# Kernel optimization log

Hardware: AMD Instinct MI355X
Metric: run time of the kernel (lower is better)

## Reference

```python
import jax, jax.numpy as jnp
import numpy as np

N_NODES = 50000
N_EDGES = 800000
F_IN, F_LAT, F_OUT = 64, 64, 64


def _graph_conv(x, W, b, src, dst, deg_out_isqrt, deg_in_isqrt):
    # DGL GraphConv, norm='both': D_out^{-1/2} scaling on src side,
    # linear transform (mult-first since in_feats >= out_feats),
    # scatter-sum to dst, D_in^{-1/2} scaling on dst side, + bias.
    n = x.shape[0]
    h = (x * deg_out_isqrt[:, None]) @ W              # [N, F_out]
    msg = h[src]                                      # [E, F_out] gather
    agg = jax.ops.segment_sum(msg, dst, num_segments=n)  # [N, F_out] scatter
    return agg * deg_in_isqrt[:, None] + b


def setup_inputs() -> dict:
    key = jax.random.key(0)
    ks = jax.random.split(key, 6)
    x = jax.random.normal(ks[0], (N_NODES, F_IN), dtype=jnp.float32)
    W1 = jax.random.normal(ks[1], (F_IN, F_LAT), dtype=jnp.float32) / np.sqrt(F_IN)
    b1 = jnp.zeros((F_LAT,), dtype=jnp.float32)
    W2 = jax.random.normal(ks[2], (F_LAT, F_OUT), dtype=jnp.float32) / np.sqrt(F_LAT)
    b2 = jnp.zeros((F_OUT,), dtype=jnp.float32)
    src = jax.random.randint(ks[3], (N_EDGES,), 0, N_NODES, dtype=jnp.int32)
    dst = jax.random.randint(ks[4], (N_EDGES,), 0, N_NODES, dtype=jnp.int32)
    return {"x": x, "W1": W1, "b1": b1, "W2": W2, "b2": b2, "src": src, "dst": dst}


def reference(x, W1, b1, W2, b2, src, dst):
    n = x.shape[0]
    ones = jnp.ones((src.shape[0],), dtype=x.dtype)
    deg_out = jax.ops.segment_sum(ones, src, num_segments=n)
    deg_in = jax.ops.segment_sum(ones, dst, num_segments=n)
    deg_out_isqrt = jnp.where(deg_out > 0, jax.lax.rsqrt(jnp.maximum(deg_out, 1.0)), 0.0)
    deg_in_isqrt = jnp.where(deg_in > 0, jax.lax.rsqrt(jnp.maximum(deg_in, 1.0)), 0.0)
    h = _graph_conv(x, W1, b1, src, dst, deg_out_isqrt, deg_in_isqrt)
    h = jax.nn.relu(h)
    out = _graph_conv(h, W2, b2, src, dst, deg_out_isqrt, deg_in_isqrt)
    return out
```

## Files before the change

### kernel.cpp

```cpp
#include <hip/hip_runtime.h>

#define NF 64
#define BC 32
#define RANGE 16384
#define RWORDS (RANGE / 4)

typedef __attribute__((ext_vector_type(8))) short short8;
typedef __attribute__((ext_vector_type(4))) float floatx4;

__device__ __forceinline__ unsigned short f2bf(float f) {
  unsigned int u = __float_as_uint(f);
  return (unsigned short)((u + 0x7fffu + ((u >> 16) & 1u)) >> 16);
}

__global__ __launch_bounds__(512) void hist_kernel(
    const int* __restrict__ src, const int* __restrict__ dst,
    unsigned char* __restrict__ Gout, unsigned char* __restrict__ Gin,
    unsigned char* __restrict__ rank, int n, int nE, int R, int chunk) {
  __shared__ int cnt[RWORDS];
  const int rb = blockIdx.x % (R * BC);
  const int kind = blockIdx.x / (R * BC);
  const int r = rb / BC, b = rb % BC;
  const int r0 = r * RANGE;
  for (int i = threadIdx.x; i < RWORDS; i += 512) cnt[i] = 0;
  __syncthreads();
  const int lo = b * chunk, hi = min(lo + chunk, nE);
  const int* keys = kind ? src : dst;
  const int n4 = (hi > lo) ? ((hi - lo) >> 2) : 0;
  const int4* keys4 = (const int4*)(keys + lo);
  if (kind == 0) {
    for (int i = threadIdx.x; i < n4; i += 512) {
      int4 v = keys4[i];
      int e0 = lo + 4 * i;
      unsigned int k, old, sh;
      k = (unsigned int)(v.x - r0);
      if (k < (unsigned int)RANGE) { sh = (k & 3) * 8; old = atomicAdd(&cnt[k >> 2], 1u << sh); rank[e0 + 0] = (unsigned char)(old >> sh); }
      k = (unsigned int)(v.y - r0);
      if (k < (unsigned int)RANGE) { sh = (k & 3) * 8; old = atomicAdd(&cnt[k >> 2], 1u << sh); rank[e0 + 1] = (unsigned char)(old >> sh); }
      k = (unsigned int)(v.z - r0);
      if (k < (unsigned int)RANGE) { sh = (k & 3) * 8; old = atomicAdd(&cnt[k >> 2], 1u << sh); rank[e0 + 2] = (unsigned char)(old >> sh); }
      k = (unsigned int)(v.w - r0);
      if (k < (unsigned int)RANGE) { sh = (k & 3) * 8; old = atomicAdd(&cnt[k >> 2], 1u << sh); rank[e0 + 3] = (unsigned char)(old >> sh); }
    }
    for (int e = lo + 4 * n4 + threadIdx.x; e < hi; e += 512) {
      unsigned int k = (unsigned int)(keys[e] - r0);
      if (k < (unsigned int)RANGE) {
        unsigned int sh = (k & 3) * 8;
        unsigned int old = atomicAdd(&cnt[k >> 2], 1u << sh);
        rank[e] = (unsigned char)(old >> sh);
      }
    }
    __syncthreads();
    unsigned int* Gw = (unsigned int*)(Gin + (size_t)b * n + r0);
    for (int i = threadIdx.x; i < RWORDS; i += 512)
      if (r0 + 4 * i < n) Gw[i] = (unsigned int)cnt[i];
  } else {
    for (int i = threadIdx.x; i < n4; i += 512) {
      int4 v = keys4[i];
      unsigned int k;
      k = (unsigned int)(v.x - r0);
      if (k < (unsigned int)RANGE) atomicAdd(&cnt[k >> 2], 1u << ((k & 3) * 8));
      k = (unsigned int)(v.y - r0);
      if (k < (unsigned int)RANGE) atomicAdd(&cnt[k >> 2], 1u << ((k & 3) * 8));
      k = (unsigned int)(v.z - r0);
      if (k < (unsigned int)RANGE) atomicAdd(&cnt[k >> 2], 1u << ((k & 3) * 8));
      k = (unsigned int)(v.w - r0);
      if (k < (unsigned int)RANGE) atomicAdd(&cnt[k >> 2], 1u << ((k & 3) * 8));
    }
    for (int e = lo + 4 * n4 + threadIdx.x; e < hi; e += 512) {
      unsigned int k = (unsigned int)(keys[e] - r0);
      if (k < (unsigned int)RANGE) atomicAdd(&cnt[k >> 2], 1u << ((k & 3) * 8));
    }
    __syncthreads();
    unsigned int* Gw = (unsigned int*)(Gout + (size_t)b * n + r0);
    for (int i = threadIdx.x; i < RWORDS; i += 512)
      if (r0 + 4 * i < n) Gw[i] = (unsigned int)cnt[i];
  }
}

__global__ __launch_bounds__(256) void colscan_scan1_kernel(
    unsigned char* __restrict__ Gin, const unsigned char* __restrict__ Gout,
    float* __restrict__ so, float* __restrict__ si,
    int* __restrict__ lscan, int* __restrict__ bsum, int n) {
  __shared__ int s[256];
  const int tid = threadIdx.x;
  const int i = blockIdx.x * 256 + tid;
  int di = 0;
  if (i < n) {
    int base = 0;
    #pragma unroll 8
    for (int b = 0; b < BC; ++b) {
      int c = Gin[(size_t)b * n + i];
      Gin[(size_t)b * n + i] = (unsigned char)base;
      base += c;
    }
    di = base;
    int dsum = 0;
    #pragma unroll 8
    for (int b = 0; b < BC; ++b) dsum += Gout[(size_t)b * n + i];
    si[i] = di > 0 ? rsqrtf((float)di) : 0.f;
    so[i] = dsum > 0 ? rsqrtf((float)dsum) : 0.f;
  }
  s[tid] = di;
  __syncthreads();
  #pragma unroll
  for (int off = 1; off < 256; off <<= 1) {
    int t2 = (tid >= off) ? s[tid - off] : 0;
    __syncthreads();
    s[tid] += t2;
    __syncthreads();
  }
  if (i < n) lscan[i] = s[tid] - di;
  if (tid == 255) bsum[blockIdx.x] = s[255];
}

__global__ __launch_bounds__(256) void scan3_basefill_kernel(
    const int* __restrict__ lscan, const int* __restrict__ bsum,
    const unsigned char* __restrict__ Gin, int* __restrict__ row_start,
    int* __restrict__ base, int n, int nb, int nE) {
  __shared__ int red[256];
  const int tid = threadIdx.x;
  const int c = blockIdx.x / nb;
  const int ib = blockIdx.x % nb;
  red[tid] = (tid < ib) ? bsum[tid] : 0;
  __syncthreads();
  #pragma unroll
  for (int s = 128; s > 0; s >>= 1) {
    if (tid < s) red[tid] += red[tid + s];
    __syncthreads();
  }
  const int off = red[0];
  const int i = ib * 256 + tid;
  if (i < n) {
    const int rs = lscan[i] + off;
    if (c == 0) row_start[i] = rs;
    base[(size_t)c * n + i] = rs + (int)Gin[(size_t)c * n + i];
  }
  if (c == 0 && ib == 0 && tid == 0) row_start[n] = nE;
}

__device__ __forceinline__ void mfma_gemm_core(
    const unsigned short* __restrict__ Ab, const unsigned short* __restrict__ Wt,
    unsigned short* __restrict__ H, int row0, int n, int t) {
  const int w = t >> 6, lane = t & 63;
  const int quad = lane >> 4, l15 = lane & 15;
  const short8 a0 = *(const short8*)&Ab[(w * 16 + l15) * 72 + quad * 8];
  const short8 a1 = *(const short8*)&Ab[(w * 16 + l15) * 72 + 32 + quad * 8];
  #pragma unroll
  for (int cg = 0; cg < 4; ++cg) {
    const short8 b0 = *(const short8*)&Wt[(cg * 16 + l15) * 72 + quad * 8];
    const short8 b1 = *(const short8*)&Wt[(cg * 16 + l15) * 72 + 32 + quad * 8];
    floatx4 acc = {0.f, 0.f, 0.f, 0.f};
    acc = __builtin_amdgcn_mfma_f32_16x16x32_bf16(a0, b0, acc, 0, 0, 0);
    acc = __builtin_amdgcn_mfma_f32_16x16x32_bf16(a1, b1, acc, 0, 0, 0);
    #pragma unroll
    for (int reg = 0; reg < 4; ++reg) {
      int grow = row0 + w * 16 + quad * 4 + reg;
      if (grow < n) H[(size_t)grow * NF + cg * 16 + l15] = f2bf(acc[reg]);
    }
  }
}

__device__ __forceinline__ void stage_wt(
    const float* __restrict__ W, unsigned short* __restrict__ Wt, int t) {
  #pragma unroll
  for (int i = 0; i < 16; ++i) {
    int idx = t + 256 * i;
    int k = idx >> 6, j = idx & 63;
    Wt[j * 72 + k] = f2bf(W[idx]);
  }
}

__global__ __launch_bounds__(256) void place_gemm1_kernel(
    const float* __restrict__ A, const float* __restrict__ so,
    const float* __restrict__ W, unsigned short* __restrict__ H, int n, int ggrid,
    const int* __restrict__ src, const int* __restrict__ dst,
    const unsigned char* __restrict__ rank, const int* __restrict__ base,
    unsigned short* __restrict__ sorted, int nE, int chunk) {
  __shared__ __align__(16) unsigned short Ab[64 * 72];
  __shared__ __align__(16) unsigned short Wt[64 * 72];
  const int t = threadIdx.x;
  if ((int)blockIdx.x >= ggrid) {
    int e = (blockIdx.x - ggrid) * 256 + t;
    if (e < nE) {
      int d = dst[e];
      int b = e / chunk;
      sorted[base[(size_t)b * n + d] + (int)rank[e]] = (unsigned short)src[e];
    }
    return;
  }
  stage_wt(W, Wt, t);
  const int row0 = blockIdx.x * 64;
  #pragma unroll
  for (int i = 0; i < 4; ++i) {
    int idx = t + 256 * i;
    int r = idx >> 4, c4 = idx & 15;
    int gr = row0 + r;
    float4 v = {0.f, 0.f, 0.f, 0.f};
    float s = 0.f;
    if (gr < n) {
      v = *(const float4*)&A[(size_t)gr * NF + c4 * 4];
      s = so[gr];
    }
    ushort4 o;
    o.x = f2bf(v.x * s); o.y = f2bf(v.y * s);
    o.z = f2bf(v.z * s); o.w = f2bf(v.w * s);
    *(ushort4*)&Ab[r * 72 + c4 * 4] = o;
  }
  __syncthreads();
  mfma_gemm_core(Ab, Wt, H, row0, n, t);
}

__device__ __forceinline__ void gather_sum(
    const unsigned short* __restrict__ H, const unsigned short* __restrict__ srcs,
    int beg, int end, int g, int c, float* acc) {
  const float4* Hv = (const float4*)H;
  int e = beg;
  for (; e + 16 <= end; e += 16) {
    int ia = srcs[e + g];
    int ib = srcs[e + 8 + g];
    float4 va = Hv[(size_t)ia * 8 + c];
    float4 vb = Hv[(size_t)ib * 8 + c];
    const unsigned int* pa = (const unsigned int*)&va;
    const unsigned int* pb = (const unsigned int*)&vb;
    #pragma unroll
    for (int k = 0; k < 4; ++k) {
      acc[2 * k]     += __uint_as_float(pa[k] << 16) + __uint_as_float(pb[k] << 16);
      acc[2 * k + 1] += __uint_as_float(pa[k] & 0xffff0000u) + __uint_as_float(pb[k] & 0xffff0000u);
    }
  }
  if (e + 8 <= end) {
    int ia = srcs[e + g];
    float4 va = Hv[(size_t)ia * 8 + c];
    const unsigned int* pa = (const unsigned int*)&va;
    #pragma unroll
    for (int k = 0; k < 4; ++k) {
      acc[2 * k]     += __uint_as_float(pa[k] << 16);
      acc[2 * k + 1] += __uint_as_float(pa[k] & 0xffff0000u);
    }
    e += 8;
  }
  if (e < end) {
    int idx = (e + g < end) ? (e + g) : (end - 1);
    float m = (e + g < end) ? 1.f : 0.f;
    int ia = srcs[idx];
    float4 va = Hv[(size_t)ia * 8 + c];
    const unsigned int* pa = (const unsigned int*)&va;
    #pragma unroll
    for (int k = 0; k < 4; ++k) {
      acc[2 * k]     += m * __uint_as_float(pa[k] << 16);
      acc[2 * k + 1] += m * __uint_as_float(pa[k] & 0xffff0000u);
    }
  }
  #pragma unroll
  for (int d = 8; d <= 32; d <<= 1) {
    #pragma unroll
    for (int k = 0; k < 8; ++k) acc[k] += __shfl_xor(acc[k], d);
  }
}

__global__ __launch_bounds__(256) void agg1_kernel(
    const unsigned short* __restrict__ H1, const int* __restrict__ row_start,
    const unsigned short* __restrict__ srcs, const float* __restrict__ si,
    const float* __restrict__ so, const float* __restrict__ b1,
    unsigned short* __restrict__ T, int n) {
  int node = blockIdx.x * 4 + (threadIdx.x >> 6);
  if (node >= n) return;
  const int lane = threadIdx.x & 63;
  const int g = lane >> 3;
  const int c = lane & 7;
  float acc[8] = {0, 0, 0, 0, 0, 0, 0, 0};
  gather_sum(H1, srcs, row_start[node], row_start[node + 1], g, c, acc);
  if (g == 0) {
    const float sin = si[node];
    const float son = so[node];
    ushort4 o0, o1;
    float v;
    v = fmaxf(fmaf(acc[0], sin, b1[c * 8 + 0]), 0.f) * son; o0.x = f2bf(v);
    v = fmaxf(fmaf(acc[1], sin, b1[c * 8 + 1]), 0.f) * son; o0.y = f2bf(v);
    v = fmaxf(fmaf(acc[2], sin, b1[c * 8 + 2]), 0.f) * son; o0.z = f2bf(v);
    v = fmaxf(fmaf(acc[3], sin, b1[c * 8 + 3]), 0.f) * son; o0.w = f2bf(v);
    v = fmaxf(fmaf(acc[4], sin, b1[c * 8 + 4]), 0.f) * son; o1.x = f2bf(v);
    v = fmaxf(fmaf(acc[5], sin, b1[c * 8 + 5]), 0.f) * son; o1.y = f2bf(v);
    v = fmaxf(fmaf(acc[6], sin, b1[c * 8 + 6]), 0.f) * son; o1.z = f2bf(v);
    v = fmaxf(fmaf(acc[7], sin, b1[c * 8 + 7]), 0.f) * son; o1.w = f2bf(v);
    *(ushort4*)&T[(size_t)node * NF + c * 8]     = o0;
    *(ushort4*)&T[(size_t)node * NF + c * 8 + 4] = o1;
  }
}

__global__ __launch_bounds__(256) void agg2_kernel(
    const unsigned short* __restrict__ Tb, const int* __restrict__ row_start,
    const unsigned short* __restrict__ srcs, const float* __restrict__ si,
    const float* __restrict__ W2, const float* __restrict__ b2,
    float* __restrict__ out, int n) {
  __shared__ __align__(16) float W2s[64 * 64];
  __shared__ float u[4][64];
  const int t = threadIdx.x;
  #pragma unroll
  for (int i = 0; i < 4; ++i)
    *(float4*)&W2s[t * 4 + 1024 * i] = *(const float4*)&W2[t * 4 + 1024 * i];
  const int w = t >> 6;
  const int lane = t & 63;
  const int g = lane >> 3;
  const int c = lane & 7;
  const int node = blockIdx.x * 4 + w;
  const bool valid = node < n;
  float acc[8] = {0, 0, 0, 0, 0, 0, 0, 0};
  if (valid) gather_sum(Tb, srcs, row_start[node], row_start[node + 1], g, c, acc);
  if (g == 0) {
    const float sin = valid ? si[node] : 0.f;
    #pragma unroll
    for (int k = 0; k < 8; ++k) u[w][c * 8 + k] = acc[k] * sin;
  }
  __syncthreads();
  if (valid) {
    float r = b2[lane];
    #pragma unroll
    for (int k = 0; k < 64; ++k) r = fmaf(u[w][k], W2s[k * 64 + lane], r);
    out[(size_t)node * NF + lane] = r;
  }
}

extern "C" void kernel_launch(void* const* d_in, const int* in_sizes, int n_in,
                              void* d_out, int out_size, void* d_ws, size_t ws_size,
                              hipStream_t stream) {
  const float* x  = (const float*)d_in[0];
  const float* W1 = (const float*)d_in[1];
  const float* b1 = (const float*)d_in[2];
  const float* W2 = (const float*)d_in[3];
  const float* b2 = (const float*)d_in[4];
  const int* src  = (const int*)d_in[5];
  const int* dst  = (const int*)d_in[6];
  float* out = (float*)d_out;

  const int N = in_sizes[0] / NF;
  const int E = in_sizes[5];
  const int NB = (N + 255) / 256;
  const int R  = (N + RANGE - 1) / RANGE;
  const int CH = (((E + BC - 1) / BC) + 3) & ~3;
  (void)ws_size;

  char* ws = (char*)d_ws;
  size_t p = 0;
  auto alloc = [&](size_t bytes) -> void* {
    void* r = ws + p;
    p = (p + bytes + 255) & ~(size_t)255;
    return r;
  };
  float* so         = (float*)alloc((size_t)N * 4);
  float* si         = (float*)alloc((size_t)N * 4);
  int*   row_start  = (int*)  alloc((size_t)(N + 1) * 4);
  int*   bsum       = (int*)  alloc((size_t)NB * 4);
  int*   lscan      = (int*)  alloc((size_t)N * 4);
  unsigned short* sorted_u16 = (unsigned short*)alloc((size_t)E * 2);
  unsigned char*  rank  = (unsigned char*)alloc((size_t)E);
  unsigned short* h1    = (unsigned short*)alloc((size_t)N * NF * 2);
  unsigned char*  G_in  = (unsigned char*)alloc((size_t)BC * N);
  unsigned char*  G_out = (unsigned char*)alloc((size_t)BC * N);
  unsigned short* tb    = (unsigned short*)alloc((size_t)N * NF * 2);
  int*            base  = (int*)alloc((size_t)BC * N * 4);

  hist_kernel<<<2 * R * BC, 512, 0, stream>>>(src, dst, G_out, G_in, rank,
                                              N, E, R, CH);

  colscan_scan1_kernel<<<NB, 256, 0, stream>>>(G_in, G_out, so, si,
                                               lscan, bsum, N);

  scan3_basefill_kernel<<<BC * NB, 256, 0, stream>>>(lscan, bsum, G_in,
                                                     row_start, base, N, NB, E);

  const int ggrid = (N + 63) / 64;
  const int pgrid = (E + 255) / 256;
  const int agrid = (N + 3) / 4;

  place_gemm1_kernel<<<ggrid + pgrid, 256, 0, stream>>>(
      x, so, W1, h1, N, ggrid, src, dst, rank, base, sorted_u16, E, CH);

  agg1_kernel<<<agrid, 256, 0, stream>>>(h1, row_start, sorted_u16, si, so, b1, tb, N);

  agg2_kernel<<<agrid, 256, 0, stream>>>(tb, row_start, sorted_u16, si, W2, b2, out, N);
}
```

Baseline: 180.9 us.

## Compute per-chunk placement bases in LDS instead of a global base array

The scan3 kernel no longer writes a BC×N int32 base array. Each placement block now rebuilds the bases for its node range in shared memory from row_start plus that chunk's Gin counts, then scans the chunk's edges, reading dst, src and rank as vectors. It writes only the edges whose destination falls in its range. The GEMM half moves to 512-thread blocks of 128 rows so both block types share one launch size. The aim is to remove about 6.4 MB of global base writes and reads, at the cost of each edge chunk being re-read once per node range (R2=4) and extra 64 KB LDS blocks that lower occupancy.

```diff
diff --git a/kernel.cpp b/kernel.cpp
--- a/kernel.cpp
+++ b/kernel.cpp
@@ -4,6 +4,8 @@
 #define BC 32
 #define RANGE 16384
 #define RWORDS (RANGE / 4)
+#define RANGE2 16384
+#define PSPLIT 4
 
 typedef __attribute__((ext_vector_type(8))) short short8;
 typedef __attribute__((ext_vector_type(4))) float floatx4;
@@ -114,15 +116,13 @@
   if (tid == 255) bsum[blockIdx.x] = s[255];
 }
 
-__global__ __launch_bounds__(256) void scan3_basefill_kernel(
+__global__ __launch_bounds__(256) void scan3_kernel(
     const int* __restrict__ lscan, const int* __restrict__ bsum,
-    const unsigned char* __restrict__ Gin, int* __restrict__ row_start,
-    int* __restrict__ base, int n, int nb, int nE) {
+    int* __restrict__ row_start, int n, int nE) {
   __shared__ int red[256];
   const int tid = threadIdx.x;
-  const int c = blockIdx.x / nb;
-  const int ib = blockIdx.x % nb;
-  red[tid] = (tid < ib) ? bsum[tid] : 0;
+  const int b = blockIdx.x;
+  red[tid] = (tid < b) ? bsum[tid] : 0;
   __syncthreads();
   #pragma unroll
   for (int s = 128; s > 0; s >>= 1) {
@@ -130,13 +130,9 @@
     __syncthreads();
   }
   const int off = red[0];
-  const int i = ib * 256 + tid;
-  if (i < n) {
-    const int rs = lscan[i] + off;
-    if (c == 0) row_start[i] = rs;
-    base[(size_t)c * n + i] = rs + (int)Gin[(size_t)c * n + i];
-  }
-  if (c == 0 && ib == 0 && tid == 0) row_start[n] = nE;
+  const int i = b * 256 + tid;
+  if (b == 0 && tid == 0) row_start[n] = nE;
+  if (i < n) row_start[i] = lscan[i] + off;
 }
 
 __device__ __forceinline__ void mfma_gemm_core(
@@ -161,54 +157,104 @@
   }
 }
 
-__device__ __forceinline__ void stage_wt(
+__device__ __forceinline__ void stage_wt512(
     const float* __restrict__ W, unsigned short* __restrict__ Wt, int t) {
   #pragma unroll
-  for (int i = 0; i < 16; ++i) {
-    int idx = t + 256 * i;
+  for (int i = 0; i < 8; ++i) {
+    int idx = t + 512 * i;
     int k = idx >> 6, j = idx & 63;
     Wt[j * 72 + k] = f2bf(W[idx]);
   }
 }
 
-__global__ __launch_bounds__(256) void place_gemm1_kernel(
+__global__ __launch_bounds__(512) void place_gemm1_kernel(
     const float* __restrict__ A, const float* __restrict__ so,
     const float* __restrict__ W, unsigned short* __restrict__ H, int n, int ggrid,
     const int* __restrict__ src, const int* __restrict__ dst,
-    const unsigned char* __restrict__ rank, const int* __restrict__ base,
+    const unsigned char* __restrict__ rank, const int* __restrict__ row_start,
+    const unsigned char* __restrict__ Gin,
     unsigned short* __restrict__ sorted, int nE, int chunk) {
-  __shared__ __align__(16) unsigned short Ab[64 * 72];
-  __shared__ __align__(16) unsigned short Wt[64 * 72];
+  __shared__ __align__(16) char smem[RANGE2 * 4];
   const int t = threadIdx.x;
   if ((int)blockIdx.x >= ggrid) {
-    int e = (blockIdx.x - ggrid) * 256 + t;
-    if (e < nE) {
-      int d = dst[e];
-      int b = e / chunk;
-      sorted[base[(size_t)b * n + d] + (int)rank[e]] = (unsigned short)src[e];
+    int* posb = (int*)smem;
+    const int pb = blockIdx.x - ggrid;
+    const int r = pb / (BC * PSPLIT);
+    const int rem = pb % (BC * PSPLIT);
+    const int b = rem / PSPLIT;
+    const int s = rem % PSPLIT;
+    const int r0 = r * RANGE2;
+    const int lim = min(RANGE2, n - r0);
+    {
+      const int4* rs4 = (const int4*)(row_start + r0);
+      const unsigned int* g4 = (const unsigned int*)(Gin + (size_t)b * n + r0);
+      int4* posb4 = (int4*)posb;
+      const int lim4 = lim >> 2;
+      for (int i = t; i < lim4; i += 512) {
+        int4 rs = rs4[i];
+        unsigned int gg = g4[i];
+        int4 o;
+        o.x = rs.x + (int)(gg & 0xffu);
+        o.y = rs.y + (int)((gg >> 8) & 0xffu);
+        o.z = rs.z + (int)((gg >> 16) & 0xffu);
+        o.w = rs.w + (int)(gg >> 24);
+        posb4[i] = o;
+      }
+    }
+    __syncthreads();
+    const int lo = b * chunk, hi = min(lo + chunk, nE);
+    const int n4 = (hi > lo) ? ((hi - lo) >> 2) : 0;
+    const int4* dst4 = (const int4*)(dst + lo);
+    const int4* src4 = (const int4*)(src + lo);
+    const unsigned int* rank4 = (const unsigned int*)(rank + lo);
+    for (int i = t + s * 512; i < n4; i += 512 * PSPLIT) {
+      int4 dv = dst4[i];
+      int4 sv = src4[i];
+      unsigned int rv = rank4[i];
+      unsigned int k;
+      k = (unsigned int)(dv.x - r0);
+      if (k < (unsigned int)lim) sorted[posb[k] + (int)(rv & 0xffu)] = (unsigned short)sv.x;
+      k = (unsigned int)(dv.y - r0);
+      if (k < (unsigned int)lim) sorted[posb[k] + (int)((rv >> 8) & 0xffu)] = (unsigned short)sv.y;
+      k = (unsigned int)(dv.z - r0);
+      if (k < (unsigned int)lim) sorted[posb[k] + (int)((rv >> 16) & 0xffu)] = (unsigned short)sv.z;
+      k = (unsigned int)(dv.w - r0);
+      if (k < (unsigned int)lim) sorted[posb[k] + (int)(rv >> 24)] = (unsigned short)sv.w;
+    }
+    if (s == 0) {
+      for (int e = lo + 4 * n4 + t; e < hi; e += 512) {
+        unsigned int k = (unsigned int)(dst[e] - r0);
+        if (k < (unsigned int)lim)
+          sorted[posb[k] + (int)rank[e]] = (unsigned short)src[e];
+      }
     }
     return;
   }
-  stage_wt(W, Wt, t);
-  const int row0 = blockIdx.x * 64;
+  unsigned short* Ab = (unsigned short*)smem;
+  unsigned short* Wt = (unsigned short*)(smem + 128 * 72 * 2);
+  stage_wt512(W, Wt, t);
+  const int row0 = blockIdx.x * 128;
   #pragma unroll
   for (int i = 0; i < 4; ++i) {
-    int idx = t + 256 * i;
+    int idx = t + 512 * i;
     int r = idx >> 4, c4 = idx & 15;
     int gr = row0 + r;
     float4 v = {0.f, 0.f, 0.f, 0.f};
-    float s = 0.f;
+    float sc = 0.f;
     if (gr < n) {
       v = *(const float4*)&A[(size_t)gr * NF + c4 * 4];
-      s = so[gr];
+      sc = so[gr];
     }
     ushort4 o;
-    o.x = f2bf(v.x * s); o.y = f2bf(v.y * s);
-    o.z = f2bf(v.z * s); o.w = f2bf(v.w * s);
+    o.x = f2bf(v.x * sc); o.y = f2bf(v.y * sc);
+    o.z = f2bf(v.z * sc); o.w = f2bf(v.w * sc);
     *(ushort4*)&Ab[r * 72 + c4 * 4] = o;
   }
   __syncthreads();
-  mfma_gemm_core(Ab, Wt, H, row0, n, t);
+  const int wid = t >> 6;
+  const int half = wid >> 2;
+  mfma_gemm_core(Ab + half * 64 * 72, Wt, H, row0 + half * 64, n,
+                 (wid & 3) * 64 + (t & 63));
 }
 
 __device__ __forceinline__ void gather_sum(
@@ -338,6 +384,7 @@
   const int E = in_sizes[5];
   const int NB = (N + 255) / 256;
   const int R  = (N + RANGE - 1) / RANGE;
+  const int R2 = (N + RANGE2 - 1) / RANGE2;
   const int CH = (((E + BC - 1) / BC) + 3) & ~3;
   (void)ws_size;
 
@@ -359,7 +406,6 @@
   unsigned char*  G_in  = (unsigned char*)alloc((size_t)BC * N);
   unsigned char*  G_out = (unsigned char*)alloc((size_t)BC * N);
   unsigned short* tb    = (unsigned short*)alloc((size_t)N * NF * 2);
-  int*            base  = (int*)alloc((size_t)BC * N * 4);
 
   hist_kernel<<<2 * R * BC, 512, 0, stream>>>(src, dst, G_out, G_in, rank,
                                               N, E, R, CH);
@@ -367,15 +413,15 @@
   colscan_scan1_kernel<<<NB, 256, 0, stream>>>(G_in, G_out, so, si,
                                                lscan, bsum, N);
 
-  scan3_basefill_kernel<<<BC * NB, 256, 0, stream>>>(lscan, bsum, G_in,
-                                                     row_start, base, N, NB, E);
-
-  const int ggrid = (N + 63) / 64;
-  const int pgrid = (E + 255) / 256;
+  scan3_kernel<<<NB, 256, 0, stream>>>(lscan, bsum, row_start, N, E);
+
+  const int ggrid = (N + 127) / 128;
+  const int pgrid = R2 * BC * PSPLIT;
   const int agrid = (N + 3) / 4;
 
-  place_gemm1_kernel<<<ggrid + pgrid, 256, 0, stream>>>(
-      x, so, W1, h1, N, ggrid, src, dst, rank, base, sorted_u16, E, CH);
+  place_gemm1_kernel<<<ggrid + pgrid, 512, 0, stream>>>(
+      x, so, W1, h1, N, ggrid, src, dst, rank, row_start, G_in,
+      sorted_u16, E, CH);
 
   agg1_kernel<<<agrid, 256, 0, stream>>>(h1, row_start, sorted_u16, si, so, b1, tb, N);
 
```

Measured after the change: 169.6 us. 1.07x faster.
